# Kernel tuning notes

Measured on AMD Instinct MI355X. Metric: run time of the kernel, lower is better.

The kernel has to match this reference:

```python
import jax, jax.numpy as jnp
import numpy as np

N, L, E, H = 8, 1024, 512, 4


def setup_inputs() -> dict:
    key = jax.random.key(0)
    ks = jax.random.split(key, 10)
    s = 1.0 / np.sqrt(E)
    return {
        "modalA": jax.random.normal(ks[0], (N, L, E), dtype=jnp.float32),
        "modalB": jax.random.normal(ks[1], (N, L, E), dtype=jnp.float32),
        "WqA": jax.random.normal(ks[2], (E, E), dtype=jnp.float32) * s,
        "bqA": jax.random.normal(ks[3], (E,), dtype=jnp.float32) * s,
        "WkA": jax.random.normal(ks[4], (E, E), dtype=jnp.float32) * s,
        "bkA": jax.random.normal(ks[5], (E,), dtype=jnp.float32) * s,
        "WqB": jax.random.normal(ks[6], (E, E), dtype=jnp.float32) * s,
        "bqB": jax.random.normal(ks[7], (E,), dtype=jnp.float32) * s,
        "WkB": jax.random.normal(ks[8], (E, E), dtype=jnp.float32) * s,
        "bkB": jax.random.normal(ks[9], (E,), dtype=jnp.float32) * s,
    }


def reference(modalA, modalB, WqA, bqA, WkA, bkA, WqB, bqB, WkB, bkB):
    # torch Linear: y = x @ W.T + b
    qA = modalA @ WqA.T + bqA  # [N, L, E]
    kA = modalA @ WkA.T + bkA
    qB = modalB @ WqB.T + bqB
    kB = modalB @ WkB.T + bkB

    # mean over heads of per-head dot products == full-dim dot / num_heads
    # (algebraically identical to einsum('nqhd,nkhd->nhqk').mean(1))
    inv_scale = 1.0 / (H * np.sqrt(E).astype(np.float32))

    def attn(q, k):
        scores = jnp.einsum('nqd,nkd->nqk', q, k) * inv_scale  # [N, L, L]
        return jax.nn.softmax(scores, axis=-1)

    weighted_A = attn(qA, kA)
    weighted_B = attn(qB, kB)
    weighted_AB = attn(qA, kB)
    weighted_BA = attn(qB, kA)

    cat_lower = jnp.concatenate([weighted_A, weighted_AB], axis=-1)  # [N, L, 2L]
    cat_upper = jnp.concatenate([weighted_B, weighted_BA], axis=-1)  # [N, L, 2L]
    cat = jnp.concatenate([cat_lower, cat_upper], axis=1)            # [N, 2L, 2L]
    return jnp.mean(cat, axis=0)                                     # [2L, 2L]
```

## Files before the change

### kernel.cpp

```cpp
#include <hip/hip_runtime.h>
#include <hip/hip_bf16.h>

typedef __bf16 bf16;
typedef bf16 bf16x8 __attribute__((ext_vector_type(8)));
typedef _Float16 f16;
typedef f16 f16x8 __attribute__((ext_vector_type(8)));
typedef float f32x4 __attribute__((ext_vector_type(4)));

constexpr int LL = 1024;
constexpr int EE = 512;
constexpr int NBATCH = 8;

__device__ __forceinline__ f32x4 mfma16(bf16x8 a, bf16x8 b, f32x4 c) {
    return __builtin_amdgcn_mfma_f32_16x16x32_bf16(a, b, c, 0, 0, 0);
}

#define GLOAD_LDS16(g, l)                                                     \
    __builtin_amdgcn_global_load_lds(                                         \
        (const __attribute__((address_space(1))) void*)(g),                   \
        (__attribute__((address_space(3))) void*)(l), 16, 0, 0)

__device__ __forceinline__ void wave_barrier() {
    __asm__ volatile("" ::: "memory");
    __builtin_amdgcn_s_barrier();
    __asm__ volatile("" ::: "memory");
}

constexpr int WAIT_VM6 = 0xF76;
constexpr int WAIT_VM0 = 0xF70;

struct CvtParams {
    const float* src[4];
    bf16* dst[4];
    int n8[4];
};

__global__ __launch_bounds__(256) void cvt_kernel(CvtParams p) {
    const int y = blockIdx.y;
    const float* __restrict__ src = p.src[y];
    bf16* __restrict__ dst = p.dst[y];
    const int n8 = p.n8[y];
    for (int i = blockIdx.x * 256 + threadIdx.x; i < n8; i += gridDim.x * 256) {
        float4 a = *(const float4*)(src + (size_t)i * 8);
        float4 b = *(const float4*)(src + (size_t)i * 8 + 4);
        bf16x8 o;
        o[0] = (bf16)a.x; o[1] = (bf16)a.y; o[2] = (bf16)a.z; o[3] = (bf16)a.w;
        o[4] = (bf16)b.x; o[5] = (bf16)b.y; o[6] = (bf16)b.z; o[7] = (bf16)b.w;
        *(bf16x8*)(dst + (size_t)i * 8) = o;
    }
}

struct ProjParams {
    const float* x[4];
    const bf16* w[4];
    const float* b[4];
};

__global__ __launch_bounds__(256, 2) void proj_kernel(ProjParams p, bf16* __restrict__ outbase) {
    const int f = blockIdx.x;
    const int xcd = f & 7;
    const int u = f >> 3;
    const int mz = xcd >> 2;
    const int by = (xcd & 3) * 16 + (u & 15);
    const int zq = (u >> 4) & 1;
    const int bxp = u >> 5;
    const int z = mz * 2 + zq;

    const float* __restrict__ X = p.x[z];
    const bf16* __restrict__ W = p.w[z];
    const float* __restrict__ Bv = p.b[z];
    bf16* __restrict__ O = outbase + (size_t)z * (NBATCH * LL) * EE;

    __shared__ union {
        struct {
            alignas(16) float Af[2][4096];
            alignas(16) bf16  Bs[2][256][32];
        } st;
        alignas(16) bf16 ep[64][264];
    } sm;

    const int t = threadIdx.x;
    const int lane = t & 63, wid = t >> 6;
    const int wm = wid & 1, wn = wid >> 1;
    const int lr = lane & 15, kg = lane >> 4;

    f32x4 acc[4][8] = {};

    const int kcT = (t >> 3) & 7;
    const int ar0 = ((t >> 6) << 3) | (t & 7);
    const float* Xst = X + (size_t)(by * 128 + ar0) * EE + kcT * 4;

    const int srow = t >> 2;
    const int cgl = t & 3;
    const int gcg = (cgl ^ ((srow >> 1) & 3)) * 8;
    const int scg = (kg ^ ((lr >> 1) & 3)) * 8;
    const bf16* Wrow0 = W + (size_t)(bxp * 256 + srow) * EE + gcg;

    auto stage = [&](int k, int b) {
        const int k0 = k * 32;
#pragma unroll
        for (int i = 0; i < 4; ++i)
            GLOAD_LDS16(Xst + (size_t)(32 * i) * EE + k0, &sm.st.Af[b][(256 * i + t) * 4]);
#pragma unroll
        for (int i = 0; i < 4; ++i)
            GLOAD_LDS16(Wrow0 + (size_t)(64 * i) * EE + k0, &sm.st.Bs[b][srow + 64 * i][cgl * 8]);
    };
    auto compute = [&](int b) {
        bf16x8 af[4], bfr[8];
#pragma unroll
        for (int im = 0; im < 4; ++im) {
            const int row = wm * 64 + im * 16 + lr;
            const int sr = ((row >> 3) << 6) + (row & 7);
            f32x4 lo = *(const f32x4*)&sm.st.Af[b][(sr + kg * 16) * 4];
            f32x4 hi = *(const f32x4*)&sm.st.Af[b][(sr + kg * 16 + 8) * 4];
#pragma unroll
            for (int e = 0; e < 4; ++e) {
                af[im][e] = (bf16)lo[e];
                af[im][4 + e] = (bf16)hi[e];
            }
        }
#pragma unroll
        for (int in = 0; in < 8; ++in)
            bfr[in] = *(const bf16x8*)&sm.st.Bs[b][wn * 128 + in * 16 + lr][scg];
#pragma unroll
        for (int im = 0; im < 4; ++im)
#pragma unroll
            for (int in = 0; in < 8; ++in)
                acc[im][in] = mfma16(af[im], bfr[in], acc[im][in]);
    };

    stage(0, 0);
#pragma unroll
    for (int k = 0; k < 16; ++k) {
        __builtin_amdgcn_s_waitcnt(WAIT_VM0);
        wave_barrier();
        if (k < 15) stage(k + 1, (k + 1) & 1);
        compute(k & 1);
    }
    __syncthreads();

#pragma unroll
    for (int pph = 0; pph < 2; ++pph) {
        if (wm == pph) {
#pragma unroll
            for (int im = 0; im < 4; ++im) {
                const int row = im * 16 + kg * 4;
#pragma unroll
                for (int in = 0; in < 8; ++in) {
                    const int col = wn * 128 + in * 16 + lr;
                    const float bias = Bv[bxp * 256 + col];
#pragma unroll
                    for (int r = 0; r < 4; ++r)
                        sm.ep[row + r][col] = (bf16)(acc[im][in][r] + bias);
                }
            }
        }
        __syncthreads();
#pragma unroll
        for (int i = 0; i < 8; ++i) {
            const int c = i * 256 + t;
            const int row = c >> 5, colg = (c & 31) * 8;
            *(uint4*)(O + (size_t)(by * 128 + pph * 64 + row) * EE + bxp * 256 + colg) =
                *(const uint4*)&sm.ep[row][colg];
        }
        __syncthreads();
    }
}

struct ScoresParams {
    const bf16* q[4];
    const bf16* k[4];
    f16* s[4];
};

__global__ __launch_bounds__(256, 2) void scores_kernel(ScoresParams p) {
    const int f = blockIdx.x;
    const int xcd = f & 7;
    const int j = f >> 3;
    const int z = (xcd << 2) + (j >> 5);
    const int map = z >> 3, n = z & 7;
    const int tile = j & 31;
    const int bxp = tile & 3, by = tile >> 2;

    const bf16* __restrict__ Qb = p.q[map] + (size_t)n * LL * EE;
    const bf16* __restrict__ Kb = p.k[map] + (size_t)n * LL * EE;
    f16* __restrict__ Sb = p.s[map] + (size_t)n * LL * LL;

    __shared__ union {
        struct { alignas(16) bf16 A[3][128][32]; alignas(16) bf16 B[3][256][32]; } st;
        alignas(16) f16 ep[64][264];
    } sm;

    const int t = threadIdx.x;
    const int lane = t & 63, wid = t >> 6;
    const int wm = wid & 1, wn = wid >> 1;
    const int lr = lane & 15, kg = lane >> 4;

    f32x4 acc[4][8] = {};

    const int srow = t >> 2;
    const int cgl = t & 3;
    const int gcg = (cgl ^ ((srow >> 1) & 3)) * 8;
    const int scg = (kg ^ ((lr >> 1) & 3)) * 8;

    const bf16* Qrow0 = Qb + (size_t)(by * 128 + srow) * EE + gcg;
    const bf16* Krow0 = Kb + (size_t)(bxp * 256 + srow) * EE + gcg;

    auto stage = [&](int k, int b) {
        const int k0 = k * 32;
#pragma unroll
        for (int i = 0; i < 2; ++i)
            GLOAD_LDS16(Qrow0 + (size_t)(64 * i) * EE + k0, &sm.st.A[b][srow + 64 * i][cgl * 8]);
#pragma unroll
        for (int i = 0; i < 4; ++i)
            GLOAD_LDS16(Krow0 + (size_t)(64 * i) * EE + k0, &sm.st.B[b][srow + 64 * i][cgl * 8]);
    };
    auto compute = [&](int b) {
        bf16x8 af[4], bfr[8];
#pragma unroll
        for (int im = 0; im < 4; ++im)
            af[im] = *(const bf16x8*)&sm.st.A[b][wm * 64 + im * 16 + lr][scg];
#pragma unroll
        for (int in = 0; in < 8; ++in)
            bfr[in] = *(const bf16x8*)&sm.st.B[b][wn * 128 + in * 16 + lr][scg];
#pragma unroll
        for (int im = 0; im < 4; ++im)
#pragma unroll
            for (int in = 0; in < 8; ++in)
                acc[im][in] = mfma16(af[im], bfr[in], acc[im][in]);
    };

    stage(0, 0);
    stage(1, 1);
#pragma unroll
    for (int k = 0; k < 16; ++k) {
        if (k < 15) __builtin_amdgcn_s_waitcnt(WAIT_VM6);
        else        __builtin_amdgcn_s_waitcnt(WAIT_VM0);
        wave_barrier();
        if (k < 14) stage(k + 2, (k + 2) % 3);
        compute(k % 3);
    }
    __syncthreads();

    const float inv_scale = 0.011048543456039806f;
#pragma unroll
    for (int pph = 0; pph < 2; ++pph) {
        if (wm == pph) {
#pragma unroll
            for (int im = 0; im < 4; ++im) {
                const int row = im * 16 + kg * 4;
#pragma unroll
                for (int in = 0; in < 8; ++in) {
                    const int col = wn * 128 + in * 16 + lr;
#pragma unroll
                    for (int r = 0; r < 4; ++r)
                        sm.ep[row + r][col] = (f16)(acc[im][in][r] * inv_scale);
                }
            }
        }
        __syncthreads();
#pragma unroll
        for (int i = 0; i < 8; ++i) {
            const int c = i * 256 + t;
            const int row = c >> 5, colg = (c & 31) * 8;
            *(uint4*)(Sb + (size_t)(by * 128 + pph * 64 + row) * LL + bxp * 256 + colg) =
                *(const uint4*)&sm.ep[row][colg];
        }
        __syncthreads();
    }
}

struct SmParams {
    const f16* s[4];
};

__global__ __launch_bounds__(256) void softmax_mean_kernel(SmParams p, float* __restrict__ out) {
    const int map = blockIdx.y;
    const f16* __restrict__ S = p.s[map];
    const int t = threadIdx.x;
    const int half = t >> 7;
    const int tl = t & 127;
    const int q = blockIdx.x * 2 + half;
    const int lane = t & 63, wid = t >> 6;
    __shared__ float red[NBATCH][4];

    f16x8 v[NBATCH];
#pragma unroll
    for (int n = 0; n < NBATCH; ++n)
        v[n] = *(const f16x8*)(S + ((size_t)n * LL + q) * LL + tl * 8);

    float e[NBATCH][8];
#pragma unroll
    for (int n = 0; n < NBATCH; ++n) {
        float s = 0.f;
#pragma unroll
        for (int j = 0; j < 8; ++j) {
            e[n][j] = __expf((float)v[n][j]);
            s += e[n][j];
        }
#pragma unroll
        for (int off = 32; off; off >>= 1) s += __shfl_xor(s, off);
        if (lane == 0) red[n][wid] = s;
    }
    __syncthreads();

    float acc[8] = {};
#pragma unroll
    for (int n = 0; n < NBATCH; ++n) {
        const float inv = 0.125f / (red[n][half * 2] + red[n][half * 2 + 1]);
#pragma unroll
        for (int j = 0; j < 8; ++j) acc[j] += e[n][j] * inv;
    }

    const int orow = (map >= 2 ? LL : 0) + q;
    const int ocol = (map & 1 ? LL : 0) + tl * 8;
    float* o = out + (size_t)orow * (2 * LL) + ocol;
    *(float4*)(o + 0) = make_float4(acc[0], acc[1], acc[2], acc[3]);
    *(float4*)(o + 4) = make_float4(acc[4], acc[5], acc[6], acc[7]);
}

extern "C" void kernel_launch(void* const* d_in, const int* in_sizes, int n_in,
                              void* d_out, int out_size, void* d_ws, size_t ws_size,
                              hipStream_t stream) {
    const float* modalA = (const float*)d_in[0];
    const float* modalB = (const float*)d_in[1];
    const float* WqA = (const float*)d_in[2];
    const float* bqA = (const float*)d_in[3];
    const float* WkA = (const float*)d_in[4];
    const float* bkA = (const float*)d_in[5];
    const float* WqB = (const float*)d_in[6];
    const float* bqB = (const float*)d_in[7];
    const float* WkB = (const float*)d_in[8];
    const float* bkB = (const float*)d_in[9];
    float* out = (float*)d_out;

    const size_t projN = (size_t)(NBATCH * LL) * EE;
    const size_t mapN = (size_t)NBATCH * LL * LL;
    char* base = (char*)d_ws;
    bf16* qk = (bf16*)base;
    char* region2 = base + 4 * projN * sizeof(bf16);
    bf16* W4 = (bf16*)region2;
    f16* S = (f16*)region2;

    CvtParams cp;
    const float* wsrc[4] = {WqA, WkA, WqB, WkB};
    for (int i = 0; i < 4; ++i) {
        cp.src[i] = wsrc[i];
        cp.dst[i] = W4 + (size_t)i * EE * EE;
        cp.n8[i] = EE * EE / 8;
    }
    cvt_kernel<<<dim3(128, 4), 256, 0, stream>>>(cp);

    ProjParams pp;
    pp.x[0] = modalA; pp.x[1] = modalA; pp.x[2] = modalB; pp.x[3] = modalB;
    for (int i = 0; i < 4; ++i) pp.w[i] = W4 + (size_t)i * EE * EE;
    pp.b[0] = bqA; pp.b[1] = bkA; pp.b[2] = bqB; pp.b[3] = bkB;
    proj_kernel<<<dim3(512), 256, 0, stream>>>(pp, qk);

    const bf16* qA = qk + 0 * projN;
    const bf16* kA = qk + 1 * projN;
    const bf16* qB = qk + 2 * projN;
    const bf16* kB = qk + 3 * projN;

    ScoresParams sp;
    sp.q[0] = qA; sp.q[1] = qA; sp.q[2] = qB; sp.q[3] = qB;
    sp.k[0] = kA; sp.k[1] = kB; sp.k[2] = kB; sp.k[3] = kA;
    for (int m = 0; m < 4; ++m) sp.s[m] = S + (size_t)m * mapN;
    scores_kernel<<<dim3(1024), 256, 0, stream>>>(sp);

    SmParams smp;
    for (int m = 0; m < 4; ++m) smp.s[m] = S + (size_t)m * mapN;
    softmax_mean_kernel<<<dim3(512, 4), 256, 0, stream>>>(smp, out);
}
```

Before: 178.4 us.

## Fuse exp and row-sum into scores epilogue, accumulate row sums atomically

The scores kernel now exponentiates the scaled scores in registers, reduces per-row partial sums across lanes, and atomically adds them into a new row-sum buffer. It stores exp values as f16 instead of raw scores. The softmax kernel then only reads the precomputed sums and does a scaled accumulation, dropping its exp, shuffle reductions and shared-memory barrier. This costs a memset, atomics, and relies on unshifted exp of small-magnitude scores staying within f16 range.

```diff
diff --git a/kernel.cpp b/kernel.cpp
--- a/kernel.cpp
+++ b/kernel.cpp
@@ -171,6 +171,7 @@
     const bf16* q[4];
     const bf16* k[4];
     f16* s[4];
+    float* rs;
 };
 
 __global__ __launch_bounds__(256, 2) void scores_kernel(ScoresParams p) {
@@ -185,6 +186,7 @@
     const bf16* __restrict__ Qb = p.q[map] + (size_t)n * LL * EE;
     const bf16* __restrict__ Kb = p.k[map] + (size_t)n * LL * EE;
     f16* __restrict__ Sb = p.s[map] + (size_t)n * LL * LL;
+    float* __restrict__ rs = p.rs + (size_t)z * LL;
 
     __shared__ union {
         struct { alignas(16) bf16 A[3][128][32]; alignas(16) bf16 B[3][256][32]; } st;
@@ -243,6 +245,24 @@
     __syncthreads();
 
     const float inv_scale = 0.011048543456039806f;
+
+#pragma unroll
+    for (int im = 0; im < 4; ++im)
+#pragma unroll
+        for (int r = 0; r < 4; ++r) {
+            float s = 0.f;
+#pragma unroll
+            for (int in = 0; in < 8; ++in) {
+                float e = __expf(acc[im][in][r] * inv_scale);
+                acc[im][in][r] = e;
+                s += e;
+            }
+            s += __shfl_xor(s, 1); s += __shfl_xor(s, 2);
+            s += __shfl_xor(s, 4); s += __shfl_xor(s, 8);
+            if (lr == 0)
+                atomicAdd(&rs[by * 128 + wm * 64 + im * 16 + kg * 4 + r], s);
+        }
+
 #pragma unroll
     for (int pph = 0; pph < 2; ++pph) {
         if (wm == pph) {
@@ -254,7 +274,7 @@
                     const int col = wn * 128 + in * 16 + lr;
 #pragma unroll
                     for (int r = 0; r < 4; ++r)
-                        sm.ep[row + r][col] = (f16)(acc[im][in][r] * inv_scale);
+                        sm.ep[row + r][col] = (f16)acc[im][in][r];
                 }
             }
         }
@@ -272,6 +292,7 @@
 
 struct SmParams {
     const f16* s[4];
+    const float* rs;
 };
 
 __global__ __launch_bounds__(256) void softmax_mean_kernel(SmParams p, float* __restrict__ out) {
@@ -281,35 +302,18 @@
     const int half = t >> 7;
     const int tl = t & 127;
     const int q = blockIdx.x * 2 + half;
-    const int lane = t & 63, wid = t >> 6;
-    __shared__ float red[NBATCH][4];
-
-    f16x8 v[NBATCH];
+
+    float inv[NBATCH];
 #pragma unroll
     for (int n = 0; n < NBATCH; ++n)
-        v[n] = *(const f16x8*)(S + ((size_t)n * LL + q) * LL + tl * 8);
-
-    float e[NBATCH][8];
+        inv[n] = 0.125f / p.rs[((size_t)(map * NBATCH + n)) * LL + q];
+
+    float acc[8] = {};
 #pragma unroll
     for (int n = 0; n < NBATCH; ++n) {
-        float s = 0.f;
-#pragma unroll
-        for (int j = 0; j < 8; ++j) {
-            e[n][j] = __expf((float)v[n][j]);
-            s += e[n][j];
-        }
-#pragma unroll
-        for (int off = 32; off; off >>= 1) s += __shfl_xor(s, off);
-        if (lane == 0) red[n][wid] = s;
-    }
-    __syncthreads();
-
-    float acc[8] = {};
-#pragma unroll
-    for (int n = 0; n < NBATCH; ++n) {
-        const float inv = 0.125f / (red[n][half * 2] + red[n][half * 2 + 1]);
-#pragma unroll
-        for (int j = 0; j < 8; ++j) acc[j] += e[n][j] * inv;
+        f16x8 v = *(const f16x8*)(S + ((size_t)n * LL + q) * LL + tl * 8);
+#pragma unroll
+        for (int j = 0; j < 8; ++j) acc[j] += (float)v[j] * inv[n];
     }
 
     const int orow = (map >= 2 ? LL : 0) + q;
@@ -341,6 +345,7 @@
     char* region2 = base + 4 * projN * sizeof(bf16);
     bf16* W4 = (bf16*)region2;
     f16* S = (f16*)region2;
+    float* rs = (float*)(region2 + 4 * mapN * sizeof(f16));
 
     CvtParams cp;
     const float* wsrc[4] = {WqA, WkA, WqB, WkB};
@@ -357,6 +362,8 @@
     pp.b[0] = bqA; pp.b[1] = bkA; pp.b[2] = bqB; pp.b[3] = bkB;
     proj_kernel<<<dim3(512), 256, 0, stream>>>(pp, qk);
 
+    hipMemsetAsync(rs, 0, (size_t)4 * NBATCH * LL * sizeof(float), stream);
+
     const bf16* qA = qk + 0 * projN;
     const bf16* kA = qk + 1 * projN;
     const bf16* qB = qk + 2 * projN;
@@ -366,9 +373,11 @@
     sp.q[0] = qA; sp.q[1] = qA; sp.q[2] = qB; sp.q[3] = qB;
     sp.k[0] = kA; sp.k[1] = kB; sp.k[2] = kB; sp.k[3] = kA;
     for (int m = 0; m < 4; ++m) sp.s[m] = S + (size_t)m * mapN;
+    sp.rs = rs;
     scores_kernel<<<dim3(1024), 256, 0, stream>>>(sp);
 
     SmParams smp;
     for (int m = 0; m < 4; ++m) smp.s[m] = S + (size_t)m * mapN;
+    smp.rs = rs;
     softmax_mean_kernel<<<dim3(512, 4), 256, 0, stream>>>(smp, out);
 }
```

Measured after the change: 185.5 us. 4.0% more time.
